# Optimization experiments

Hardware: AMD Instinct MI355X
Metric: run time of the kernel (lower is better)

## Reference

```python
import jax, jax.numpy as jnp
import numpy as np

B, L, H = 64, 1024, 1024


def setup_inputs() -> dict:
    key = jax.random.key(0)
    k1, k2, k3, k4 = jax.random.split(key, 4)
    scale = 1.0 / np.sqrt(H)
    return {
        "hidden": jax.random.normal(k1, (1, B, H), dtype=jnp.float32),
        "encoder_outputs": jax.random.normal(k2, (L, B, H), dtype=jnp.float32),
        "W": jax.random.normal(k3, (H, H), dtype=jnp.float32) * scale,
        "b": jax.random.normal(k4, (H,), dtype=jnp.float32) * scale,
    }


def reference(hidden, encoder_outputs, W, b):
    # 'general' Luong attention: e[b, i] = hidden_b . (W @ enc_{i,b} + b)
    # torch nn.Linear(x) = x @ W.T + b
    proj = jnp.einsum("lbh,gh->lbg", encoder_outputs, W) + b  # [L, B, H]
    energies = jnp.einsum("bh,lbh->bl", hidden[0], proj)       # [B, L]
    a_ij = jax.nn.softmax(energies, axis=1)[:, None, :]        # [B, 1, L]
    return a_ij
```

## Files before the change

### kernel.cpp

```cpp
#include <hip/hip_runtime.h>

#define H 1024
#define B 64
#define L 1024

__global__ __launch_bounds__(256) void proj_hidden_kernel(
    const float* __restrict__ hidden,
    const float* __restrict__ W,
    float* __restrict__ v) {
    __shared__ float sh[H];
    const int bid   = blockIdx.x;
    const int b     = bid >> 2;
    const int chunk = bid & 3;
    const int tid   = threadIdx.x;

    for (int i = tid; i < H; i += 256) sh[i] = hidden[b * H + i];
    __syncthreads();

    const int h = chunk * 256 + tid;
    float acc = 0.f;
#pragma unroll 8
    for (int g = 0; g < H; ++g) {
        acc += sh[g] * W[(size_t)g * H + h];
    }
    v[b * H + h] = acc;
}

__global__ __launch_bounds__(256) void energy_kernel(
    const float* __restrict__ enc,
    const float* __restrict__ v,
    float* __restrict__ e) {
    const int wave = (blockIdx.x * 256 + threadIdx.x) >> 6;
    const int lane = threadIdx.x & 63;
    const int b = wave & (B - 1);
    const int l = wave >> 6;

    const float4* __restrict__ ep =
        reinterpret_cast<const float4*>(enc + ((size_t)l * B + b) * H);
    const float4* __restrict__ vp =
        reinterpret_cast<const float4*>(v + (size_t)b * H);

    float acc = 0.f;
#pragma unroll
    for (int k = 0; k < 4; ++k) {
        float4 a = ep[lane + k * 64];
        float4 w = vp[lane + k * 64];
        acc += a.x * w.x + a.y * w.y + a.z * w.z + a.w * w.w;
    }
#pragma unroll
    for (int off = 32; off; off >>= 1) acc += __shfl_down(acc, off, 64);
    if (lane == 0) e[(size_t)b * L + l] = acc;
}

__global__ __launch_bounds__(1024) void softmax_kernel(
    const float* __restrict__ e,
    float* __restrict__ out) {
    const int b = blockIdx.x;
    const int tid = threadIdx.x;
    const int wid = tid >> 6, lane = tid & 63;
    __shared__ float red[16];

    float x = e[(size_t)b * L + tid];

    float m = x;
#pragma unroll
    for (int off = 32; off; off >>= 1) m = fmaxf(m, __shfl_down(m, off, 64));
    if (lane == 0) red[wid] = m;
    __syncthreads();
    if (tid < 16) {
        float t = red[tid];
#pragma unroll
        for (int off = 8; off; off >>= 1) t = fmaxf(t, __shfl_down(t, off, 16));
        if (tid == 0) red[0] = t;
    }
    __syncthreads();
    m = red[0];
    __syncthreads();

    float ex = __expf(x - m);
    float s = ex;
#pragma unroll
    for (int off = 32; off; off >>= 1) s += __shfl_down(s, off, 64);
    if (lane == 0) red[wid] = s;
    __syncthreads();
    if (tid < 16) {
        float t = red[tid];
#pragma unroll
        for (int off = 8; off; off >>= 1) t += __shfl_down(t, off, 16);
        if (tid == 0) red[0] = t;
    }
    __syncthreads();
    s = red[0];

    out[(size_t)b * L + tid] = ex / s;
}

extern "C" void kernel_launch(void* const* d_in, const int* in_sizes, int n_in,
                              void* d_out, int out_size, void* d_ws, size_t ws_size,
                              hipStream_t stream) {
    const float* hidden = (const float*)d_in[0];
    const float* enc    = (const float*)d_in[1];
    const float* W      = (const float*)d_in[2];
    float* out = (float*)d_out;

    float* v = (float*)d_ws;
    float* e = v + (size_t)B * H;

    proj_hidden_kernel<<<B * (H / 256), 256, 0, stream>>>(hidden, W, v);
    energy_kernel<<<(B * L * 64) / 256, 256, 0, stream>>>(enc, v, e);
    softmax_kernel<<<B, 1024, 0, stream>>>(e, out);
}
```

Baseline: 429.6 us.

## Split-K the hidden projection and batch four rows per wave in energy

The projection kernel now gives each block 64 output columns and splits the 1024-long reduction across four wave segments, combining the partial sums through shared memory. This launches four times as many blocks to raise parallelism in the small GEMV. The energy kernel now loads the v vector into registers once per wave and reuses it across four sequence positions, and it reads the encoder stream with nontemporal loads to avoid polluting the cache. Together these cut redundant v loads and give more loads in flight, at the cost of more registers per wave and fewer waves overall.

```diff
diff --git a/kernel.cpp b/kernel.cpp
--- a/kernel.cpp
+++ b/kernel.cpp
@@ -4,26 +4,38 @@
 #define B 64
 #define L 1024
 
+typedef float vf4 __attribute__((ext_vector_type(4)));
+
 __global__ __launch_bounds__(256) void proj_hidden_kernel(
     const float* __restrict__ hidden,
     const float* __restrict__ W,
     float* __restrict__ v) {
     __shared__ float sh[H];
-    const int bid   = blockIdx.x;
-    const int b     = bid >> 2;
-    const int chunk = bid & 3;
-    const int tid   = threadIdx.x;
+    __shared__ float part[4][64];
+    const int bid = blockIdx.x;
+    const int b   = bid >> 4;
+    const int h0  = (bid & 15) << 6;
+    const int tid = threadIdx.x;
+    const int hl  = tid & 63;
+    const int seg = tid >> 6;
 
     for (int i = tid; i < H; i += 256) sh[i] = hidden[b * H + i];
     __syncthreads();
 
-    const int h = chunk * 256 + tid;
+    const int h = h0 + hl;
+    const float* __restrict__ Wp = W + (size_t)(seg * 256) * H + h;
+    const float* __restrict__ sp = sh + seg * 256;
     float acc = 0.f;
 #pragma unroll 8
-    for (int g = 0; g < H; ++g) {
-        acc += sh[g] * W[(size_t)g * H + h];
+    for (int g = 0; g < 256; ++g) {
+        acc += sp[g] * Wp[(size_t)g * H];
     }
-    v[b * H + h] = acc;
+    part[seg][hl] = acc;
+    __syncthreads();
+    if (tid < 64) {
+        v[b * H + h0 + tid] =
+            part[0][tid] + part[1][tid] + part[2][tid] + part[3][tid];
+    }
 }
 
 __global__ __launch_bounds__(256) void energy_kernel(
@@ -32,24 +44,35 @@
     float* __restrict__ e) {
     const int wave = (blockIdx.x * 256 + threadIdx.x) >> 6;
     const int lane = threadIdx.x & 63;
-    const int b = wave & (B - 1);
-    const int l = wave >> 6;
+    const int b  = wave & (B - 1);
+    const int l0 = (wave >> 6) << 2;
 
-    const float4* __restrict__ ep =
-        reinterpret_cast<const float4*>(enc + ((size_t)l * B + b) * H);
-    const float4* __restrict__ vp =
-        reinterpret_cast<const float4*>(v + (size_t)b * H);
+    const vf4* __restrict__ vp = reinterpret_cast<const vf4*>(v + (size_t)b * H);
+    const vf4 w0 = vp[lane], w1 = vp[lane + 64], w2 = vp[lane + 128], w3 = vp[lane + 192];
 
-    float acc = 0.f;
+    float acc[4];
 #pragma unroll
-    for (int k = 0; k < 4; ++k) {
-        float4 a = ep[lane + k * 64];
-        float4 w = vp[lane + k * 64];
-        acc += a.x * w.x + a.y * w.y + a.z * w.z + a.w * w.w;
+    for (int j = 0; j < 4; ++j) {
+        const vf4* __restrict__ ep =
+            reinterpret_cast<const vf4*>(enc + ((size_t)(l0 + j) * B + b) * H);
+        vf4 a0 = __builtin_nontemporal_load(ep + lane);
+        vf4 a1 = __builtin_nontemporal_load(ep + lane + 64);
+        vf4 a2 = __builtin_nontemporal_load(ep + lane + 128);
+        vf4 a3 = __builtin_nontemporal_load(ep + lane + 192);
+        acc[j] = a0.x * w0.x + a0.y * w0.y + a0.z * w0.z + a0.w * w0.w
+               + a1.x * w1.x + a1.y * w1.y + a1.z * w1.z + a1.w * w1.w
+               + a2.x * w2.x + a2.y * w2.y + a2.z * w2.z + a2.w * w2.w
+               + a3.x * w3.x + a3.y * w3.y + a3.z * w3.z + a3.w * w3.w;
     }
 #pragma unroll
-    for (int off = 32; off; off >>= 1) acc += __shfl_down(acc, off, 64);
-    if (lane == 0) e[(size_t)b * L + l] = acc;
+    for (int off = 32; off; off >>= 1) {
+#pragma unroll
+        for (int j = 0; j < 4; ++j) acc[j] += __shfl_down(acc[j], off, 64);
+    }
+    if (lane == 0) {
+#pragma unroll
+        for (int j = 0; j < 4; ++j) e[(size_t)b * L + l0 + j] = acc[j];
+    }
 }
 
 __global__ __launch_bounds__(1024) void softmax_kernel(
@@ -106,7 +129,7 @@
     float* v = (float*)d_ws;
     float* e = v + (size_t)B * H;
 
-    proj_hidden_kernel<<<B * (H / 256), 256, 0, stream>>>(hidden, W, v);
-    energy_kernel<<<(B * L * 64) / 256, 256, 0, stream>>>(enc, v, e);
+    proj_hidden_kernel<<<B * (H / 64), 256, 0, stream>>>(hidden, W, v);
+    energy_kernel<<<(B * L / 4) / 4, 256, 0, stream>>>(enc, v, e);
     softmax_kernel<<<B, 1024, 0, stream>>>(e, out);
 }
```

New measurement: 360.6 us. 1.19x faster.
